# Kernel optimization log

Hardware: AMD Instinct MI355X
Metric: run time of the kernel (lower is better)

The kernel has to match this reference:

```python
import jax, jax.numpy as jnp
import numpy as np

B, N, S, D1, D2 = 8, 16384, 1024, 256, 256
C_IN, C_MID, C_OUT = D1 + D2, 256, 256
BN_EPS = 1e-5
DIST_EPS = 1e-8


def setup_inputs() -> dict:
    key = jax.random.key(0)
    ks = jax.random.split(key, 12)
    return {
        "xyz1": jax.random.normal(ks[0], (B, 3, N), jnp.float32),
        "xyz2": jax.random.normal(ks[1], (B, 3, S), jnp.float32),
        "points1": jax.random.normal(ks[2], (B, D1, N), jnp.float32),
        "points2": jax.random.normal(ks[3], (B, D2, S), jnp.float32),
        "w0": jax.random.normal(ks[4], (C_MID, C_IN), jnp.float32) * (1.0 / np.sqrt(C_IN)),
        "b0": jnp.zeros((C_MID,), jnp.float32),
        "g0": jnp.ones((C_MID,), jnp.float32),
        "be0": jnp.zeros((C_MID,), jnp.float32),
        "w1": jax.random.normal(ks[5], (C_OUT, C_MID), jnp.float32) * (1.0 / np.sqrt(C_MID)),
        "b1": jnp.zeros((C_OUT,), jnp.float32),
        "g1": jnp.ones((C_OUT,), jnp.float32),
        "be1": jnp.zeros((C_OUT,), jnp.float32),
    }


def _propagate(xyz1, xyz2, points1, points2):
    # xyz1 [B,3,N], xyz2 [B,3,S], points1 [B,D1,N], points2 [B,D2,S]
    x1 = jnp.transpose(xyz1, (0, 2, 1))   # [B,N,3]
    x2 = jnp.transpose(xyz2, (0, 2, 1))   # [B,S,3]
    p2 = jnp.transpose(points2, (0, 2, 1))  # [B,S,D2]
    # squared pairwise distances [B,N,S]
    d = (jnp.sum(x1 * x1, -1, keepdims=True)
         - 2.0 * jnp.einsum('bnc,bsc->bns', x1, x2)
         + jnp.sum(x2 * x2, -1)[:, None, :])
    neg_d, idx = jax.lax.top_k(-d, 3)     # 3 nearest neighbors
    dist = -neg_d                          # [B,N,3]
    recip = 1.0 / (dist + DIST_EPS)
    w = recip / jnp.sum(recip, -1, keepdims=True)  # [B,N,3]
    gathered = jax.vmap(lambda feats, ids: feats[ids])(p2, idx)  # [B,N,3,D2]
    interp = jnp.sum(gathered * w[..., None], axis=2)            # [B,N,D2]
    p1 = jnp.transpose(points1, (0, 2, 1))  # [B,N,D1]
    new = jnp.concatenate([p1, interp], axis=-1)  # [B,N,D1+D2]
    return jnp.transpose(new, (0, 2, 1))          # [B,C_IN,N]


def _conv_bn_relu(x, w, b, g, be):
    # 1x1 conv as matmul; BN in training mode (batch stats over B and N)
    y = jnp.einsum('oc,bcn->bon', w, x) + b[None, :, None]
    mean = jnp.mean(y, axis=(0, 2), keepdims=True)
    var = jnp.var(y, axis=(0, 2), keepdims=True)
    y = (y - mean) * jax.lax.rsqrt(var + BN_EPS)
    y = y * g[None, :, None] + be[None, :, None]
    return jax.nn.relu(y)


def reference(xyz1, xyz2, points1, points2, w0, b0, g0, be0, w1, b1, g1, be1):
    x = _propagate(xyz1, xyz2, points1, points2)  # [B,512,N]
    x = _conv_bn_relu(x, w0, b0, g0, be0)
    x = _conv_bn_relu(x, w1, b1, g1, be1)
    return x  # [B,256,N]
```

## Files before the change

kernel.cpp:

```cpp
#include <hip/hip_runtime.h>
#include <stdint.h>

#define BB    8
#define NN_   16384
#define SS    1024
#define PP    131072
#define CIN   512
#define CMID  256
#define COUT  256

typedef short  bf16x8 __attribute__((ext_vector_type(8)));
typedef float  f32x4  __attribute__((ext_vector_type(4)));
typedef unsigned short u16x8 __attribute__((ext_vector_type(8)));
typedef unsigned int uint_;

__device__ __forceinline__ float bf2f(unsigned short u){
  union { unsigned int i; float f; } v; v.i = ((unsigned int)u) << 16; return v.f;
}
__device__ __forceinline__ unsigned short f2bf(float f){
  union { float f; unsigned int i; } v; v.f = f;
  unsigned int r = (v.i + 0x7fffu + ((v.i >> 16) & 1u)) >> 16;
  return (unsigned short)r;
}

__device__ __forceinline__ void async_ld16(const void* g, void* l){
  const uint32_t __attribute__((address_space(1)))* gp =
    reinterpret_cast<const uint32_t __attribute__((address_space(1)))*>(reinterpret_cast<uintptr_t>(g));
  uint32_t __attribute__((address_space(3)))* lp =
    reinterpret_cast<uint32_t __attribute__((address_space(3)))*>(reinterpret_cast<uintptr_t>(l));
  __builtin_amdgcn_global_load_lds(gp, lp, 16, 0, 0);
}

__global__ void k_prep(const float* __restrict__ w0, const float* __restrict__ w1,
                       unsigned short* __restrict__ w0b, unsigned short* __restrict__ w1b,
                       float* __restrict__ bn)
{
  int idx = blockIdx.x * 256 + threadIdx.x;
  if (idx < 131072) w0b[idx] = f2bf(w0[idx]);
  if (idx < 65536)  w1b[idx] = f2bf(w1[idx]);
  if (idx < 2048)   bn[idx]  = 0.0f;
}

__global__ void k_p2t(const float* __restrict__ p2, float* __restrict__ p2t)
{
  __shared__ float t[32][33];
  const int b = blockIdx.z, c0 = blockIdx.y * 32, s0 = blockIdx.x * 32;
  const int tx = threadIdx.x, ty = threadIdx.y;
#pragma unroll
  for (int r = 0; r < 4; r++)
    t[ty + r*8][tx] = p2[((size_t)b*256 + c0 + ty + r*8) * SS + s0 + tx];
  __syncthreads();
#pragma unroll
  for (int r = 0; r < 4; r++)
    p2t[((size_t)b*SS + s0 + ty + r*8) * 256 + c0 + tx] = t[tx][ty + r*8];
}

__global__ void k_p1t(const float* __restrict__ p1, unsigned short* __restrict__ xcat)
{
  __shared__ float t[32][33];
  const int b = blockIdx.z, c0 = blockIdx.y * 32, n0 = blockIdx.x * 32;
  const int tx = threadIdx.x, ty = threadIdx.y;
#pragma unroll
  for (int r = 0; r < 4; r++)
    t[ty + r*8][tx] = p1[((size_t)b*256 + c0 + ty + r*8) * (size_t)NN_ + n0 + tx];
  __syncthreads();
#pragma unroll
  for (int r = 0; r < 4; r++)
    xcat[((size_t)b*NN_ + n0 + ty + r*8) * 512 + c0 + tx] = f2bf(t[tx][ty + r*8]);
}

__global__ __launch_bounds__(256) void k_nn(const float* __restrict__ xyz1,
                                            const float* __restrict__ xyz2,
                                            const float* __restrict__ p2t,
                                            unsigned short* __restrict__ xcat)
{
  __shared__ float4 pts[SS];
  __shared__ int4   mi[256];
  __shared__ float4 mw[256];
  const int blk = blockIdx.x;
  const int b = blk & 7, nt = blk >> 3;
  const int n0 = nt * 256, tid = threadIdx.x;

  for (int s = tid; s < SS; s += 256) {
    float x = xyz2[((size_t)b*3 + 0) * SS + s];
    float y = xyz2[((size_t)b*3 + 1) * SS + s];
    float z = xyz2[((size_t)b*3 + 2) * SS + s];
    pts[s] = make_float4(x, y, z, 0.0f);
  }
  __syncthreads();

  const int n = n0 + tid;
  const float qx = xyz1[((size_t)b*3 + 0) * NN_ + n];
  const float qy = xyz1[((size_t)b*3 + 1) * NN_ + n];
  const float qz = xyz1[((size_t)b*3 + 2) * NN_ + n];

  const float KINIT = __uint_as_float(0x7F7FFFFFu);
  float c0 = KINIT, c1 = KINIT, c2 = KINIT, c3 = KINIT, c4 = KINIT, c5 = KINIT;
#pragma unroll 4
  for (int s = 0; s < SS; s++) {
    float4 p = pts[s];
    float dx = qx - p.x, dy = qy - p.y, dz = qz - p.z;
    float d = fmaf(dx, dx, fmaf(dy, dy, dz * dz));
    float key = __uint_as_float((__float_as_uint(d) & 0xFFFFFC00u) | (uint_)s);
    float m0 = fminf(c0, key);
    float m1 = __builtin_amdgcn_fmed3f(c0, c1, key);
    float m2 = __builtin_amdgcn_fmed3f(c1, c2, key);
    float m3 = __builtin_amdgcn_fmed3f(c2, c3, key);
    float m4 = __builtin_amdgcn_fmed3f(c3, c4, key);
    float m5 = __builtin_amdgcn_fmed3f(c4, c5, key);
    c0 = m0; c1 = m1; c2 = m2; c3 = m3; c4 = m4; c5 = m5;
  }

  const double qxd = (double)qx, qyd = (double)qy, qzd = (double)qz;
  uint_  ks[6] = { __float_as_uint(c0), __float_as_uint(c1), __float_as_uint(c2),
                   __float_as_uint(c3), __float_as_uint(c4), __float_as_uint(c5) };
  int    ii[6];
  double dd[6];
#pragma unroll
  for (int t = 0; t < 6; t++) {
    ii[t] = (int)(ks[t] & 1023u);
    float4 p = pts[ii[t]];
    double dx = qxd - (double)p.x, dy = qyd - (double)p.y, dz = qzd - (double)p.z;
    dd[t] = dx*dx + dy*dy + dz*dz;
  }
#pragma unroll
  for (int a = 1; a < 6; a++)
#pragma unroll
    for (int c = a; c > 0; c--)
      if (dd[c] < dd[c-1]) {
        double td = dd[c]; dd[c] = dd[c-1]; dd[c-1] = td;
        int    ti = ii[c]; ii[c] = ii[c-1]; ii[c-1] = ti;
      }

  double r0 = 1.0/(dd[0] + 1e-8), r1 = 1.0/(dd[1] + 1e-8), r2 = 1.0/(dd[2] + 1e-8);
  double rs = 1.0/(r0 + r1 + r2);
  mi[tid] = make_int4(ii[0], ii[1], ii[2], 0);
  mw[tid] = make_float4((float)(r0*rs), (float)(r1*rs), (float)(r2*rs), 0.0f);
  __syncthreads();

  const int wid = tid >> 6, lane = tid & 63;
  const float* p2tb = p2t + (size_t)b * SS * 256;
  unsigned short* outb = xcat + ((size_t)b*NN_ + n0) * 512 + 256 + lane*4;
#pragma unroll 2
  for (int t = 0; t < 64; t++) {
    int j = wid*64 + t;
    int4   im = mi[j];
    float4 wm = mw[j];
    const float4* ra = (const float4*)(p2tb + (size_t)im.x * 256) + lane;
    const float4* rb = (const float4*)(p2tb + (size_t)im.y * 256) + lane;
    const float4* rc = (const float4*)(p2tb + (size_t)im.z * 256) + lane;
    float4 A = *ra, Bv = *rb, Cv = *rc;
    float fx = wm.x*A.x + wm.y*Bv.x + wm.z*Cv.x;
    float fy = wm.x*A.y + wm.y*Bv.y + wm.z*Cv.y;
    float fz = wm.x*A.z + wm.y*Bv.z + wm.z*Cv.z;
    float fw = wm.x*A.w + wm.y*Bv.w + wm.z*Cv.w;
    uint_ lo = (uint_)f2bf(fx) | ((uint_)f2bf(fy) << 16);
    uint_ hi = (uint_)f2bf(fz) | ((uint_)f2bf(fw) << 16);
    uint2 pk; pk.x = lo; pk.y = hi;
    *(uint2*)(outb + (size_t)j * 512) = pk;
  }
}

__global__ __launch_bounds__(512, 2) void k_gemm(const unsigned short* __restrict__ X,
                                                 const unsigned short* __restrict__ W,
                                                 unsigned short* __restrict__ Y,
                                                 float* __restrict__ bnsum,
                                                 float* __restrict__ bnsumsq,
                                                 int K)
{
  extern __shared__ char smem[];
  const int tid  = threadIdx.x;
  const int wid  = tid >> 6, lane = tid & 63;
  const int quad = lane >> 4, l16 = lane & 15;
  const int wp = wid >> 2, wo = wid & 3;
  const size_t p0 = (size_t)blockIdx.x * 256;

  f32x4 acc[8][4] = {};

  const int grow = (wid << 4) | (lane >> 2);
  const int gcol = (((lane & 3) ^ ((lane >> 3) & 3)) << 3);
  const unsigned short* gA0 = X + (p0 + grow)       * (size_t)K + gcol;
  const unsigned short* gA1 = X + (p0 + grow + 128) * (size_t)K + gcol;
  const unsigned short* gB0 = W + (size_t)(grow)       * K + gcol;
  const unsigned short* gB1 = W + (size_t)(grow + 128) * K + gcol;
  const int ldw = wid << 10;

  auto stage = [&](int t) {
    char* base = smem + ((t & 3) << 15);
    const int kk = t << 5;
    async_ld16(gA0 + kk, base + ldw);
    async_ld16(gA1 + kk, base + 8192 + ldw);
    async_ld16(gB0 + kk, base + 16384 + ldw);
    async_ld16(gB1 + kk, base + 16384 + 8192 + ldw);
  };

  const int sw   = (quad ^ ((l16 >> 1) & 3)) << 4;
  const int aoff = ((wp << 7) + l16) * 64 + sw;
  const int boff = ((wo << 6) + l16) * 64 + sw;

  const int nt = K >> 5;
  stage(0); stage(1); stage(2);
  asm volatile("s_waitcnt vmcnt(8)" ::: "memory");
  __builtin_amdgcn_s_barrier();

  for (int t = 0; t < nt; ++t) {
    if (t + 3 < nt) stage(t + 3);
    const char* buf = smem + ((t & 3) << 15);
    bf16x8 af[8], bfr[4];
#pragma unroll
    for (int m = 0; m < 8; m++) af[m]  = *(const bf16x8*)(buf + aoff + m*1024);
#pragma unroll
    for (int n = 0; n < 4; n++) bfr[n] = *(const bf16x8*)(buf + 16384 + boff + n*1024);
    __builtin_amdgcn_s_setprio(1);
#pragma unroll
    for (int m = 0; m < 8; m++)
#pragma unroll
      for (int n = 0; n < 4; n++)
        acc[m][n] = __builtin_amdgcn_mfma_f32_16x16x32_bf16(af[m], bfr[n], acc[m][n], 0, 0, 0);
    __builtin_amdgcn_s_setprio(0);
    if (t < nt - 1) {
      if (t + 3 < nt)       asm volatile("s_waitcnt vmcnt(8)" ::: "memory");
      else if (t + 3 == nt) asm volatile("s_waitcnt vmcnt(4)" ::: "memory");
      else                  asm volatile("s_waitcnt vmcnt(0)" ::: "memory");
      __builtin_amdgcn_s_barrier();
    }
  }

#pragma unroll
  for (int n = 0; n < 4; n++) {
    float s = 0.0f, ss = 0.0f;
#pragma unroll
    for (int m = 0; m < 8; m++)
#pragma unroll
      for (int i = 0; i < 4; i++) { float v = acc[m][n][i]; s += v; ss += v*v; }
    s  += __shfl_xor(s, 16, 64);  s  += __shfl_xor(s, 32, 64);
    ss += __shfl_xor(ss, 16, 64); ss += __shfl_xor(ss, 32, 64);
    if (quad == 0) {
      int o = (wo << 6) + (n << 4) + l16;
      atomicAdd(&bnsum[o], s);
      atomicAdd(&bnsumsq[o], ss);
    }
  }
#pragma unroll
  for (int m = 0; m < 8; m++)
#pragma unroll
    for (int n = 0; n < 4; n++)
#pragma unroll
      for (int i = 0; i < 4; i++) {
        size_t p = p0 + (wp << 7) + (m << 4) + (quad << 2) + i;
        int    o = (wo << 6) + (n << 4) + l16;
        Y[p * 256 + o] = f2bf(acc[m][n][i]);
      }
}

__global__ void k_bn(const float* __restrict__ sum, const float* __restrict__ sumsq,
                     const float* __restrict__ g, const float* __restrict__ be,
                     float* __restrict__ scale, float* __restrict__ shift)
{
  int o = threadIdx.x;
  const float inv = 1.0f / 131072.0f;
  float m  = sum[o] * inv;
  float v  = sumsq[o] * inv - m * m;
  float sc = g[o] * rsqrtf(v + 1e-5f);
  scale[o] = sc;
  shift[o] = be[o] - m * sc;
}

__global__ __launch_bounds__(256) void k_z(const unsigned short* __restrict__ y,
                                           const float* __restrict__ scale,
                                           const float* __restrict__ shift,
                                           unsigned short* __restrict__ z)
{
  size_t idx = ((size_t)blockIdx.x * 256 + threadIdx.x) * 8;
  int o = (int)(idx & 255);
  u16x8 v = *(const u16x8*)(y + idx);
  u16x8 r;
#pragma unroll
  for (int i = 0; i < 8; i++) {
    float f = bf2f(v[i]);
    float t = f * scale[o + i] + shift[o + i];
    r[i] = f2bf(fmaxf(t, 0.0f));
  }
  *(u16x8*)(z + idx) = r;
}

__global__ __launch_bounds__(256) void k_out(const unsigned short* __restrict__ y1,
                                             const float* __restrict__ scale,
                                             const float* __restrict__ shift,
                                             float* __restrict__ out)
{
  __shared__ float t[64][65];
  const int b = blockIdx.z, o0 = blockIdx.y * 64, n0 = blockIdx.x * 64;
  const int tx = threadIdx.x & 15, ty = threadIdx.x >> 4;
  const float4 sc = *(const float4*)(scale + o0 + tx*4);
  const float4 sh = *(const float4*)(shift + o0 + tx*4);
#pragma unroll
  for (int r = 0; r < 4; r++) {
    int nl = ty + r*16;
    const unsigned short* src = y1 + ((size_t)b*NN_ + n0 + nl) * 256 + o0 + tx*4;
    ushort4 v = *(const ushort4*)src;
    t[tx*4+0][nl] = fmaxf(bf2f(v.x) * sc.x + sh.x, 0.0f);
    t[tx*4+1][nl] = fmaxf(bf2f(v.y) * sc.y + sh.y, 0.0f);
    t[tx*4+2][nl] = fmaxf(bf2f(v.z) * sc.z + sh.z, 0.0f);
    t[tx*4+3][nl] = fmaxf(bf2f(v.w) * sc.w + sh.w, 0.0f);
  }
  __syncthreads();
#pragma unroll
  for (int r = 0; r < 4; r++) {
    int ol = ty + r*16;
    float4 o4 = make_float4(t[ol][tx*4+0], t[ol][tx*4+1], t[ol][tx*4+2], t[ol][tx*4+3]);
    *(float4*)(out + ((size_t)b*256 + o0 + ol) * (size_t)NN_ + n0 + tx*4) = o4;
  }
}

extern "C" void kernel_launch(void* const* d_in, const int* in_sizes, int n_in,
                              void* d_out, int out_size, void* d_ws, size_t ws_size,
                              hipStream_t stream)
{
  const float* xyz1 = (const float*)d_in[0];
  const float* xyz2 = (const float*)d_in[1];
  const float* p1   = (const float*)d_in[2];
  const float* p2   = (const float*)d_in[3];
  const float* w0   = (const float*)d_in[4];
  const float* g0   = (const float*)d_in[6];
  const float* be0  = (const float*)d_in[7];
  const float* w1   = (const float*)d_in[8];
  const float* g1   = (const float*)d_in[10];
  const float* be1  = (const float*)d_in[11];

  char* ws = (char*)d_ws;
  unsigned short* xcat = (unsigned short*)(ws);
  unsigned short* y0   = (unsigned short*)(ws + 134217728ull);
  unsigned short* zbuf = (unsigned short*)(ws);
  unsigned short* y1   = (unsigned short*)(ws + 67108864ull);
  float*          p2t  = (float*)        (ws + 134217728ull);
  unsigned short* w0b  = (unsigned short*)(ws + 201326592ull);
  unsigned short* w1b  = (unsigned short*)(ws + 201588736ull);
  float*          bn   = (float*)        (ws + 201719808ull);

  static bool s_init = false;
  if (!s_init) {
    hipFuncSetAttribute(reinterpret_cast<const void*>(&k_gemm),
                        hipFuncAttributeMaxDynamicSharedMemorySize, 131072);
    s_init = true;
  }

  k_prep<<<512, 256, 0, stream>>>(w0, w1, w0b, w1b, bn);
  k_p2t <<<dim3(32, 8, 8),  dim3(32, 8), 0, stream>>>(p2, p2t);
  k_p1t <<<dim3(512, 8, 8), dim3(32, 8), 0, stream>>>(p1, xcat);
  k_nn  <<<512, 256, 0, stream>>>(xyz1, xyz2, p2t, xcat);
  k_gemm<<<512, 512, 131072, stream>>>(xcat, w0b, y0, bn + 0,   bn + 256, 512);
  k_bn  <<<1, 256, 0, stream>>>(bn + 0,   bn + 256, g0, be0, bn + 1024, bn + 1280);
  k_z   <<<16384, 256, 0, stream>>>(y0, bn + 1024, bn + 1280, zbuf);
  k_gemm<<<512, 512, 131072, stream>>>(zbuf, w1b, y1, bn + 512, bn + 768, 256);
  k_bn  <<<1, 256, 0, stream>>>(bn + 512, bn + 768, g1, be1, bn + 1536, bn + 1792);
  k_out <<<dim3(256, 4, 8), 256, 0, stream>>>(y1, bn + 1536, bn + 1792, (float*)d_out);
}
```

Baseline: 505.7 us.

## Fuse BN+ReLU of first layer into second GEMM's A-operand load; expand kNN distance

Removes the standalone k_z elementwise pass by applying the layer-0 BN scale/shift and ReLU to A fragments after they are read from LDS in the second GEMM. The per-channel parameters are staged into extra shared memory. This saves a full read and write of the 64MB intermediate, but adds VALU work in the MFMA loop, and the larger LDS footprint may affect the 2-blocks-per-CU occupancy. Separately, the kNN distance is rewritten as |q|^2 - 2q·p + |p|^2 with |p|^2 precomputed, which can change rounding and neighbor ordering.

```diff
diff --git a/kernel.cpp b/kernel.cpp
--- a/kernel.cpp
+++ b/kernel.cpp
@@ -85,7 +85,7 @@
     float x = xyz2[((size_t)b*3 + 0) * SS + s];
     float y = xyz2[((size_t)b*3 + 1) * SS + s];
     float z = xyz2[((size_t)b*3 + 2) * SS + s];
-    pts[s] = make_float4(x, y, z, 0.0f);
+    pts[s] = make_float4(x, y, z, fmaf(x, x, fmaf(y, y, z * z)));
   }
   __syncthreads();
 
@@ -93,14 +93,15 @@
   const float qx = xyz1[((size_t)b*3 + 0) * NN_ + n];
   const float qy = xyz1[((size_t)b*3 + 1) * NN_ + n];
   const float qz = xyz1[((size_t)b*3 + 2) * NN_ + n];
+  const float qx2 = -2.0f*qx, qy2 = -2.0f*qy, qz2 = -2.0f*qz;
+  const float qq  = fmaf(qx, qx, fmaf(qy, qy, qz * qz));
 
   const float KINIT = __uint_as_float(0x7F7FFFFFu);
   float c0 = KINIT, c1 = KINIT, c2 = KINIT, c3 = KINIT, c4 = KINIT, c5 = KINIT;
 #pragma unroll 4
   for (int s = 0; s < SS; s++) {
     float4 p = pts[s];
-    float dx = qx - p.x, dy = qy - p.y, dz = qz - p.z;
-    float d = fmaf(dx, dx, fmaf(dy, dy, dz * dz));
+    float d = fmaf(qx2, p.x, fmaf(qy2, p.y, fmaf(qz2, p.z, p.w))) + qq;
     float key = __uint_as_float((__float_as_uint(d) & 0xFFFFFC00u) | (uint_)s);
     float m0 = fminf(c0, key);
     float m1 = __builtin_amdgcn_fmed3f(c0, c1, key);
@@ -161,12 +162,15 @@
   }
 }
 
+template<bool FUSE>
 __global__ __launch_bounds__(512, 2) void k_gemm(const unsigned short* __restrict__ X,
                                                  const unsigned short* __restrict__ W,
                                                  unsigned short* __restrict__ Y,
                                                  float* __restrict__ bnsum,
                                                  float* __restrict__ bnsumsq,
-                                                 int K)
+                                                 int K,
+                                                 const float* __restrict__ zscale,
+                                                 const float* __restrict__ zshift)
 {
   extern __shared__ char smem[];
   const int tid  = threadIdx.x;
@@ -174,6 +178,7 @@
   const int quad = lane >> 4, l16 = lane & 15;
   const int wp = wid >> 2, wo = wid & 3;
   const size_t p0 = (size_t)blockIdx.x * 256;
+  float* pprm = (float*)(smem + 131072);
 
   f32x4 acc[8][4] = {};
 
@@ -198,8 +203,16 @@
   const int aoff = ((wp << 7) + l16) * 64 + sw;
   const int boff = ((wo << 6) + l16) * 64 + sw;
 
+  float psc = 0.0f, psh = 0.0f;
+  if constexpr (FUSE) {
+    if (tid < 256) { psc = zscale[tid]; psh = zshift[tid]; }
+  }
   const int nt = K >> 5;
   stage(0); stage(1); stage(2);
+  if constexpr (FUSE) {
+    if (tid < 256) { pprm[tid] = psc; pprm[256 + tid] = psh; }
+    asm volatile("s_waitcnt lgkmcnt(0)" ::: "memory");
+  }
   asm volatile("s_waitcnt vmcnt(8)" ::: "memory");
   __builtin_amdgcn_s_barrier();
 
@@ -211,6 +224,21 @@
     for (int m = 0; m < 8; m++) af[m]  = *(const bf16x8*)(buf + aoff + m*1024);
 #pragma unroll
     for (int n = 0; n < 4; n++) bfr[n] = *(const bf16x8*)(buf + 16384 + boff + n*1024);
+    if constexpr (FUSE) {
+      const float* sp = pprm + (t << 5) + (quad << 3);
+      f32x4 sc0 = *(const f32x4*)sp,         sc1 = *(const f32x4*)(sp + 4);
+      f32x4 sh0 = *(const f32x4*)(sp + 256), sh1 = *(const f32x4*)(sp + 260);
+#pragma unroll
+      for (int m = 0; m < 8; m++) {
+#pragma unroll
+        for (int j = 0; j < 8; j++) {
+          float f  = bf2f((unsigned short)af[m][j]);
+          float s_ = (j < 4) ? sc0[j] : sc1[j - 4];
+          float h_ = (j < 4) ? sh0[j] : sh1[j - 4];
+          af[m][j] = (short)f2bf(fmaxf(fmaf(f, s_, h_), 0.0f));
+        }
+      }
+    }
     __builtin_amdgcn_s_setprio(1);
 #pragma unroll
     for (int m = 0; m < 8; m++)
@@ -264,24 +292,6 @@
   float sc = g[o] * rsqrtf(v + 1e-5f);
   scale[o] = sc;
   shift[o] = be[o] - m * sc;
-}
-
-__global__ __launch_bounds__(256) void k_z(const unsigned short* __restrict__ y,
-                                           const float* __restrict__ scale,
-                                           const float* __restrict__ shift,
-                                           unsigned short* __restrict__ z)
-{
-  size_t idx = ((size_t)blockIdx.x * 256 + threadIdx.x) * 8;
-  int o = (int)(idx & 255);
-  u16x8 v = *(const u16x8*)(y + idx);
-  u16x8 r;
-#pragma unroll
-  for (int i = 0; i < 8; i++) {
-    float f = bf2f(v[i]);
-    float t = f * scale[o + i] + shift[o + i];
-    r[i] = f2bf(fmaxf(t, 0.0f));
-  }
-  *(u16x8*)(z + idx) = r;
 }
 
 __global__ __launch_bounds__(256) void k_out(const unsigned short* __restrict__ y1,
@@ -331,7 +341,6 @@
   char* ws = (char*)d_ws;
   unsigned short* xcat = (unsigned short*)(ws);
   unsigned short* y0   = (unsigned short*)(ws + 134217728ull);
-  unsigned short* zbuf = (unsigned short*)(ws);
   unsigned short* y1   = (unsigned short*)(ws + 67108864ull);
   float*          p2t  = (float*)        (ws + 134217728ull);
   unsigned short* w0b  = (unsigned short*)(ws + 201326592ull);
@@ -340,8 +349,10 @@
 
   static bool s_init = false;
   if (!s_init) {
-    hipFuncSetAttribute(reinterpret_cast<const void*>(&k_gemm),
+    hipFuncSetAttribute(reinterpret_cast<const void*>(&k_gemm<false>),
                         hipFuncAttributeMaxDynamicSharedMemorySize, 131072);
+    hipFuncSetAttribute(reinterpret_cast<const void*>(&k_gemm<true>),
+                        hipFuncAttributeMaxDynamicSharedMemorySize, 133120);
     s_init = true;
   }
 
@@ -349,10 +360,11 @@
   k_p2t <<<dim3(32, 8, 8),  dim3(32, 8), 0, stream>>>(p2, p2t);
   k_p1t <<<dim3(512, 8, 8), dim3(32, 8), 0, stream>>>(p1, xcat);
   k_nn  <<<512, 256, 0, stream>>>(xyz1, xyz2, p2t, xcat);
-  k_gemm<<<512, 512, 131072, stream>>>(xcat, w0b, y0, bn + 0,   bn + 256, 512);
+  k_gemm<false><<<512, 512, 131072, stream>>>(xcat, w0b, y0, bn + 0, bn + 256, 512,
+                                              nullptr, nullptr);
   k_bn  <<<1, 256, 0, stream>>>(bn + 0,   bn + 256, g0, be0, bn + 1024, bn + 1280);
-  k_z   <<<16384, 256, 0, stream>>>(y0, bn + 1024, bn + 1280, zbuf);
-  k_gemm<<<512, 512, 131072, stream>>>(zbuf, w1b, y1, bn + 512, bn + 768, 256);
+  k_gemm<true><<<512, 512, 133120, stream>>>(y0, w1b, y1, bn + 512, bn + 768, 256,
+                                             bn + 1024, bn + 1280);
   k_bn  <<<1, 256, 0, stream>>>(bn + 512, bn + 768, g1, be1, bn + 1536, bn + 1792);
   k_out <<<dim3(256, 4, 8), 256, 0, stream>>>(y1, bn + 1536, bn + 1792, (float*)d_out);
 }
```

Measured after the change: 497.7 us. About the same (-1.6%).
